# Kernel tuning notes

Hardware: AMD Instinct MI355X
Metric: run time of the kernel (lower is better)

The kernel has to match this reference:

```python
import jax, jax.numpy as jnp
import numpy as np

RAY_START, RAY_END, BOX_SIZE = 0.0, 1.0, 2.0
EPS = 1e-10


def grid_sample_bilinear(img, grid):
    """Replicates F.grid_sample(mode='bilinear', padding_mode='zeros', align_corners=True).
    img: [N, F, H, W]; grid: [N, P, 2] with (x, y) in [-1, 1] (x indexes W, y indexes H).
    Returns [N, F, P]."""
    H, W = img.shape[2], img.shape[3]
    x = (grid[..., 0] + 1.0) * 0.5 * (W - 1)  # [N, P]
    y = (grid[..., 1] + 1.0) * 0.5 * (H - 1)
    x0 = jnp.floor(x).astype(jnp.int32)
    y0 = jnp.floor(y).astype(jnp.int32)
    x1, y1 = x0 + 1, y0 + 1
    wx = x - x0.astype(x.dtype)
    wy = y - y0.astype(y.dtype)

    def gather(ix, iy):
        valid = ((ix >= 0) & (ix < W) & (iy >= 0) & (iy < H)).astype(img.dtype)
        ixc = jnp.clip(ix, 0, W - 1)
        iyc = jnp.clip(iy, 0, H - 1)
        v = jax.vmap(lambda im, jx, jy: im[:, jy, jx])(img, ixc, iyc)  # [N, F, P]
        return v * valid[:, None, :]

    return (gather(x0, y0) * ((1 - wx) * (1 - wy))[:, None, :]
            + gather(x1, y0) * (wx * (1 - wy))[:, None, :]
            + gather(x0, y1) * ((1 - wx) * wy)[:, None, :]
            + gather(x1, y1) * (wx * wy)[:, None, :])


def setup_inputs() -> dict:
    key = jax.random.key(0)
    ks = jax.random.split(key, 6)
    B, R, N, F, HP, HID = 2, 4096, 48, 32, 256, 64
    planes = jax.random.normal(ks[0], (B, 3, F, HP, HP), jnp.float32)
    ray_origins = jax.random.normal(ks[1], (B, R, 3), jnp.float32) * 0.05
    rd = jax.random.normal(ks[2], (B, R, 3), jnp.float32)
    ray_directions = rd / jnp.linalg.norm(rd, axis=-1, keepdims=True)
    jitter = jax.random.uniform(ks[3], (B, R, N, 1), jnp.float32)
    W1 = jax.random.normal(ks[4], (F, HID), jnp.float32) * 0.1
    b1 = jnp.zeros((HID,), jnp.float32)
    W2 = jax.random.normal(ks[5], (HID, 4), jnp.float32) * 0.1
    b2 = jnp.zeros((4,), jnp.float32)
    return dict(planes=planes, ray_origins=ray_origins, ray_directions=ray_directions,
                jitter=jitter, W1=W1, b1=b1, W2=W2, b2=b2)


def reference(planes, ray_origins, ray_directions, jitter, W1, b1, W2, b2):
    B, R, N, _ = jitter.shape
    F_, HP, WP = planes.shape[2], planes.shape[3], planes.shape[4]
    P = R * N

    # sample_stratified over normalized s in [0, 1], jittered (EG3D style)
    steps = jnp.arange(N, dtype=jnp.float32) / (N - 1)          # [N]
    s_delta = 1.0 / (N - 1)
    sdist = steps.reshape(1, 1, N, 1) + jitter * s_delta         # [B, R, N, 1]
    tdist = sdist * RAY_END + (1.0 - sdist) * RAY_START          # s_to_t

    # world-space sample coordinates -> tri-plane lookup
    coords = ray_origins[:, :, None, :] + tdist * ray_directions[:, :, None, :]  # [B,R,N,3]
    coords = coords.reshape(B, P, 3) / (BOX_SIZE / 2.0)
    c2d = jnp.stack([coords[..., (0, 1)], coords[..., (0, 2)], coords[..., (1, 2)]],
                    axis=1).reshape(B * 3, P, 2)
    feats = grid_sample_bilinear(planes.reshape(B * 3, F_, HP, WP), c2d)  # [B*3, F, P]
    feats = feats.reshape(B, 3, F_, P).transpose(0, 1, 3, 2)              # [B, 3, P, F]

    # OSGDecoder-style MLP: mean over planes, Linear -> softplus -> Linear
    x = feats.mean(axis=1)                      # [B, P, F]
    h = jax.nn.softplus(x @ W1 + b1)            # [B, P, HID]
    o = h @ W2 + b2                             # [B, P, 4]
    sigma = o[..., :1].reshape(B, R, N, 1)
    rgb = (jax.nn.sigmoid(o[..., 1:]) * 1.002 - 0.001).reshape(B, R, N, 3)

    # ClassicalRayMarcher (clamp_mode='softplus', cut_quantile=0, use_inf_depth=True)
    deltas = sdist[:, :, 1:] - sdist[:, :, :-1]
    deltas = jnp.concatenate([deltas, jnp.full_like(deltas[:, :, :1], 1e10)], axis=2)
    dens = jax.nn.softplus(sigma)
    alphas = 1.0 - jnp.exp(-deltas * dens)                     # [B, R, N, 1]
    T = jnp.cumprod(1.0 - alphas + EPS, axis=2)
    T = jnp.concatenate([jnp.ones_like(T[:, :, :1]), T], axis=2)  # [B, R, N+1, 1]
    final_transmittance = T[:, :, -1, 0]                       # [B, R]
    weights = alphas * T[:, :, :-1]                            # [B, R, N, 1]
    rgb_final = jnp.sum(weights * rgb, axis=2)                 # [B, R, 3]
    depth = jnp.sum(weights * sdist, axis=2)                   # [B, R, 1]
    return rgb_final, depth, weights.sum(axis=2), final_transmittance
```

## Files before the change

kernel.cpp:

```cpp
#include <hip/hip_runtime.h>
#include <math.h>

#define BATCH 2
#define RAYS  4096
#define NS    48
#define FEAT  32
#define HP    256
#define HID   64
#define NRAY  (BATCH*RAYS)
#define NSAMP (NRAY*NS)
#define S_DELTA (1.0f/47.0f)

typedef unsigned short u16;
typedef __attribute__((ext_vector_type(8))) short bfrag8;
typedef __attribute__((ext_vector_type(4))) float facc4;

__device__ __forceinline__ float softplus_f(float t) {
    float e = __expf(-fabsf(t));
    return fmaxf(t, 0.0f) + __logf(1.0f + e);
}
__device__ __forceinline__ float sigmoid_f(float t) {
    return 1.0f / (1.0f + __expf(-t));
}
__device__ __forceinline__ unsigned rtne16(float f) {
    unsigned u = __float_as_uint(f);
    return (u + 0x7FFFu + ((u >> 16) & 1u)) >> 16;
}

__global__ __launch_bounds__(256)
void prep_kernel(const float* __restrict__ planes,
                 const float* __restrict__ W1,
                 const float* __restrict__ W2,
                 u16* __restrict__ pT,
                 u16* __restrict__ W1F,
                 u16* __restrict__ W2F) {
    int idx = blockIdx.x * 256 + threadIdx.x;
    const int total = BATCH * 3 * HP * HP;
    if (idx < total) {
        int xy = idx % (HP * HP);
        int bp = idx / (HP * HP);
        const float* src = planes + (size_t)bp * FEAT * HP * HP + xy;
        unsigned o16[16];
        #pragma unroll
        for (int k = 0; k < 16; ++k) {
            float v0 = src[(size_t)(2 * k) * HP * HP];
            float v1 = src[(size_t)(2 * k + 1) * HP * HP];
            o16[k] = rtne16(v0) | (rtne16(v1) << 16);
        }
        uint4* dst = (uint4*)(pT + (size_t)idx * FEAT);
        #pragma unroll
        for (int q = 0; q < 4; ++q)
            dst[q] = make_uint4(o16[4*q], o16[4*q+1], o16[4*q+2], o16[4*q+3]);
    } else {
        int r = idx - total;
        #pragma unroll
        for (int i = 0; i < 8; ++i) {
            int e = r * 8 + i;
            int nt = e >> 9, ll = (e >> 3) & 63, ii = e & 7;
            int k = ((ll >> 4) << 3) + ii;
            int nn = (nt << 4) + (ll & 15);
            W1F[e] = (u16)rtne16(W1[k * HID + nn]);
        }
        if (r < 128) {
            #pragma unroll
            for (int i = 0; i < 8; ++i) {
                int e = r * 8 + i;
                int kk = e >> 9, ll = (e >> 3) & 63, ii = e & 7;
                int k = kk * 32 + ((ll >> 4) << 3) + ii;
                int nn = ll & 15;
                W2F[e] = (nn < 4) ? (u16)rtne16(W2[k * 4 + nn]) : (u16)0;
            }
        }
    }
}

__device__ __forceinline__ void corner_bf16(const u16* __restrict__ p,
                                            float w, float acc[8]) {
    uint4 q = *(const uint4*)p;
    unsigned uu[4] = {q.x, q.y, q.z, q.w};
    #pragma unroll
    for (int i = 0; i < 4; ++i) {
        float lo = __uint_as_float(uu[i] << 16);
        float hi = __uint_as_float(uu[i] & 0xFFFF0000u);
        acc[2*i]   = fmaf(w, lo, acc[2*i]);
        acc[2*i+1] = fmaf(w, hi, acc[2*i+1]);
    }
}

__device__ __forceinline__ void gather_plane_bf16(const u16* __restrict__ pb,
                                                  float gx, float gy, int fc8,
                                                  float acc[8]) {
    float px = (gx + 1.0f) * 0.5f * (float)(HP - 1);
    float py = (gy + 1.0f) * 0.5f * (float)(HP - 1);
    float fx = floorf(px), fy = floorf(py);
    float wx = px - fx, wy = py - fy;
    int x0 = (int)fx, y0 = (int)fy;
    int x1 = x0 + 1, y1 = y0 + 1;
    bool vx0 = (unsigned)x0 < HP, vx1 = (unsigned)x1 < HP;
    bool vy0 = (unsigned)y0 < HP, vy1 = (unsigned)y1 < HP;
    int cx0 = min(max(x0, 0), HP-1), cx1 = min(max(x1, 0), HP-1);
    int cy0 = min(max(y0, 0), HP-1), cy1 = min(max(y1, 0), HP-1);
    float w00 = (vx0 && vy0) ? (1.f-wx)*(1.f-wy) : 0.f;
    float w10 = (vx1 && vy0) ? wx*(1.f-wy)       : 0.f;
    float w01 = (vx0 && vy1) ? (1.f-wx)*wy       : 0.f;
    float w11 = (vx1 && vy1) ? wx*wy             : 0.f;
    corner_bf16(pb + ((size_t)(cy0*HP + cx0)*FEAT + fc8), w00, acc);
    corner_bf16(pb + ((size_t)(cy0*HP + cx1)*FEAT + fc8), w10, acc);
    corner_bf16(pb + ((size_t)(cy1*HP + cx0)*FEAT + fc8), w01, acc);
    corner_bf16(pb + ((size_t)(cy1*HP + cx1)*FEAT + fc8), w11, acc);
}

__global__ __launch_bounds__(256)
void sample_mlp_mfma(const u16* __restrict__ pT,
                     const float* __restrict__ rayo,
                     const float* __restrict__ rayd,
                     const float* __restrict__ jitter,
                     const u16* __restrict__ W1F,
                     const u16* __restrict__ W2F,
                     const float* __restrict__ b1,
                     const float* __restrict__ b2,
                     float4* __restrict__ smp, float* __restrict__ sds) {
    __shared__ __align__(16) u16 hlds[4][1024];
    const int t = threadIdx.x;
    const int w = t >> 6;
    const int l = t & 63;
    const int c = l & 15;
    const int g = l >> 4;
    const int sbase = (blockIdx.x * 4 + w) * 16;
    const int s = sbase + c;
    const int ray = s / NS;
    const int n = s - ray * NS;
    const int b = ray >> 12;

    const float jit = jitter[s];
    const float sd = fmaf((float)n, S_DELTA, jit * S_DELTA);
    const float ox = rayo[ray*3+0], oy = rayo[ray*3+1], oz = rayo[ray*3+2];
    const float dx = rayd[ray*3+0], dy = rayd[ray*3+1], dz = rayd[ray*3+2];
    const float cxv = fmaf(sd, dx, ox);
    const float cyv = fmaf(sd, dy, oy);
    const float czv = fmaf(sd, dz, oz);

    float acc[8];
    #pragma unroll
    for (int i = 0; i < 8; ++i) acc[i] = 0.f;

    const int fc8 = g * 8;
    const u16* base = pT + (size_t)b * 3 * HP * HP * FEAT;
    gather_plane_bf16(base,                         cxv, cyv, fc8, acc);
    gather_plane_bf16(base + (size_t)HP*HP*FEAT,    cxv, czv, fc8, acc);
    gather_plane_bf16(base + 2*(size_t)HP*HP*FEAT,  cyv, czv, fc8, acc);

    union { unsigned u[4]; bfrag8 v; } A;
    #pragma unroll
    for (int p = 0; p < 4; ++p)
        A.u[p] = rtne16(acc[2*p] * (1.f/3.f)) |
                 (rtne16(acc[2*p+1] * (1.f/3.f)) << 16);

    const facc4 z4 = {0.f, 0.f, 0.f, 0.f};
    facc4 H[4];
    #pragma unroll
    for (int nt = 0; nt < 4; ++nt) {
        union { uint4 q; bfrag8 v; } B;
        B.q = *(const uint4*)(W1F + (size_t)(nt * 64 + l) * 8);
        H[nt] = __builtin_amdgcn_mfma_f32_16x16x32_bf16(A.v, B.v, z4, 0, 0, 0);
    }

    char* lb = (char*)&hlds[w][0];
    #pragma unroll
    for (int nt = 0; nt < 4; ++nt) {
        const float bb = b1[nt * 16 + c];
        #pragma unroll
        for (int r = 0; r < 4; ++r) {
            const int row = g * 4 + r;
            const float hv = softplus_f(H[nt][r] + bb);
            const int off = row * 128 + ((((nt * 16 + c) * 2)) ^ ((row & 7) << 4));
            *(u16*)(lb + off) = (u16)rtne16(hv);
        }
    }

    facc4 O = z4;
    #pragma unroll
    for (int kk = 0; kk < 2; ++kk) {
        union { uint4 q; bfrag8 v; } A2;
        const int off = c * 128 + ((kk * 64 + g * 16) ^ ((c & 7) << 4));
        A2.q = *(const uint4*)(lb + off);
        union { uint4 q; bfrag8 v; } B2;
        B2.q = *(const uint4*)(W2F + (size_t)(kk * 64 + l) * 8);
        O = __builtin_amdgcn_mfma_f32_16x16x32_bf16(A2.v, B2.v, O, 0, 0, 0);
    }

    if (c < 4) {
        const float bb = b2[c];
        #pragma unroll
        for (int r = 0; r < 4; ++r) {
            const int ss = sbase + g * 4 + r;
            const float o = O[r] + bb;
            const float val = (c == 0) ? softplus_f(o)
                                       : (sigmoid_f(o) * 1.002f - 0.001f);
            ((float*)&smp[ss])[c] = val;
        }
    }
    if (g == 0) sds[s] = sd;
}

__global__ __launch_bounds__(256)
void composite(const float4* __restrict__ smp, const float* __restrict__ sds,
               float* __restrict__ out) {
    int w    = threadIdx.x >> 6;
    int lane = threadIdx.x & 63;
    int ray  = blockIdx.x * 4 + w;
    int base = ray * NS;
    bool valid = lane < NS;

    float4 v = make_float4(0.f, 0.f, 0.f, 0.f);
    float sd = 0.f;
    if (valid) { v = smp[base + lane]; sd = sds[base + lane]; }
    float sdn = __shfl_down(sd, 1);

    float alpha = 0.f, l = 0.f;
    if (valid) {
        float delta = (lane < NS - 1) ? (sdn - sd) : 1e10f;
        float tt = __expf(-delta * v.x);
        alpha = 1.0f - tt;
        l = __logf(tt + 1e-10f);
    }
    float sacc = l;
    #pragma unroll
    for (int off = 1; off < 64; off <<= 1) {
        float u = __shfl_up(sacc, off);
        if (lane >= off) sacc += u;
    }
    float finalLog = __shfl(sacc, NS - 1);
    float T   = __expf(sacc - l);
    float wgt = valid ? alpha * T : 0.f;

    float rf = wgt * v.y, gf = wgt * v.z, bf = wgt * v.w;
    float dep = wgt * sd, wsum = wgt;
    #pragma unroll
    for (int off = 32; off; off >>= 1) {
        rf   += __shfl_xor(rf, off);
        gf   += __shfl_xor(gf, off);
        bf   += __shfl_xor(bf, off);
        dep  += __shfl_xor(dep, off);
        wsum += __shfl_xor(wsum, off);
    }
    if (lane == 0) {
        out[ray * 3 + 0] = rf;
        out[ray * 3 + 1] = gf;
        out[ray * 3 + 2] = bf;
        out[NRAY * 3 + ray] = dep;
        out[NRAY * 4 + ray] = wsum;
        out[NRAY * 5 + ray] = __expf(finalLog);
    }
}

__global__ __launch_bounds__(192)
void render_fused(const float* __restrict__ pl,
                  const float* __restrict__ rayo,
                  const float* __restrict__ rayd,
                  const float* __restrict__ jitter,
                  const float* __restrict__ W1, const float* __restrict__ b1,
                  const float* __restrict__ W2, const float* __restrict__ b2,
                  float* __restrict__ out) {
    __shared__ float4 smpb[192];
    __shared__ float  sdsb[192];
    int tid = threadIdx.x;
    int lr  = tid / NS;
    int n   = tid - lr * NS;
    int ray = blockIdx.x * 4 + lr;
    int b   = ray >> 12;

    float jit = jitter[ray * NS + n];
    float sd  = (float)n * S_DELTA + jit * S_DELTA;
    float ox = rayo[ray*3+0], oy = rayo[ray*3+1], oz = rayo[ray*3+2];
    float dx = rayd[ray*3+0], dy = rayd[ray*3+1], dz = rayd[ray*3+2];
    float cx = fmaf(sd, dx, ox), cy = fmaf(sd, dy, oy), cz = fmaf(sd, dz, oz);

    float xv[32];
    #pragma unroll
    for (int i = 0; i < 32; ++i) xv[i] = 0.f;
    const size_t psz = (size_t)HP * HP * FEAT;
    const float* base = pl + (size_t)b * 3 * psz;
    float gxs[3] = {cx, cx, cy}, gys[3] = {cy, cz, cz};
    for (int p = 0; p < 3; ++p) {
        float px = (gxs[p] + 1.0f) * 0.5f * (float)(HP - 1);
        float py = (gys[p] + 1.0f) * 0.5f * (float)(HP - 1);
        float fx = floorf(px), fy = floorf(py);
        float wx = px - fx, wy = py - fy;
        int x0 = (int)fx, y0 = (int)fy, x1 = x0 + 1, y1 = y0 + 1;
        const float* pb = base + p * psz;
        float ws[4] = {(1.f-wx)*(1.f-wy), wx*(1.f-wy), (1.f-wx)*wy, wx*wy};
        int xs[4] = {x0, x1, x0, x1}, ys[4] = {y0, y0, y1, y1};
        for (int q = 0; q < 4; ++q) {
            if ((unsigned)xs[q] < HP && (unsigned)ys[q] < HP) {
                const float* pp = pb + (size_t)ys[q] * HP + xs[q];
                #pragma unroll
                for (int f = 0; f < 32; ++f)
                    xv[f] = fmaf(ws[q], pp[(size_t)f * HP * HP], xv[f]);
            }
        }
    }
    #pragma unroll
    for (int i = 0; i < 32; ++i) xv[i] *= (1.f/3.f);

    float o0 = b2[0], o1 = b2[1], o2 = b2[2], o3 = b2[3];
    #pragma unroll
    for (int j = 0; j < HID; ++j) {
        float hj = b1[j];
        #pragma unroll
        for (int f = 0; f < FEAT; ++f) hj = fmaf(xv[f], W1[f * HID + j], hj);
        hj = softplus_f(hj);
        o0 = fmaf(hj, W2[j*4+0], o0);
        o1 = fmaf(hj, W2[j*4+1], o1);
        o2 = fmaf(hj, W2[j*4+2], o2);
        o3 = fmaf(hj, W2[j*4+3], o3);
    }
    smpb[tid] = make_float4(softplus_f(o0),
                            sigmoid_f(o1) * 1.002f - 0.001f,
                            sigmoid_f(o2) * 1.002f - 0.001f,
                            sigmoid_f(o3) * 1.002f - 0.001f);
    sdsb[tid] = sd;
    __syncthreads();

    if (tid < 4) {
        int rray = blockIdx.x * 4 + tid;
        const float4* sp  = &smpb[tid * NS];
        const float*  sdp = &sdsb[tid * NS];
        float T = 1.0f, rf = 0.f, gf = 0.f, bfv = 0.f, dep = 0.f, wsum = 0.f;
        for (int m = 0; m < NS; ++m) {
            float4 vv = sp[m];
            float sdc = sdp[m];
            float delta = (m < NS - 1) ? (sdp[m+1] - sdc) : 1e10f;
            float alpha = 1.0f - __expf(-delta * vv.x);
            float wq = alpha * T;
            rf = fmaf(wq, vv.y, rf);
            gf = fmaf(wq, vv.z, gf);
            bfv = fmaf(wq, vv.w, bfv);
            dep = fmaf(wq, sdc, dep);
            wsum += wq;
            T *= (1.0f - alpha + 1e-10f);
        }
        out[rray*3+0] = rf;
        out[rray*3+1] = gf;
        out[rray*3+2] = bfv;
        out[NRAY*3 + rray] = dep;
        out[NRAY*4 + rray] = wsum;
        out[NRAY*5 + rray] = T;
    }
}

extern "C" void kernel_launch(void* const* d_in, const int* in_sizes, int n_in,
                              void* d_out, int out_size, void* d_ws, size_t ws_size,
                              hipStream_t stream) {
    const float* planes = (const float*)d_in[0];
    const float* rayo   = (const float*)d_in[1];
    const float* rayd   = (const float*)d_in[2];
    const float* jitter = (const float*)d_in[3];
    const float* W1     = (const float*)d_in[4];
    const float* b1     = (const float*)d_in[5];
    const float* W2     = (const float*)d_in[6];
    const float* b2     = (const float*)d_in[7];
    float* out = (float*)d_out;

    const size_t pT_bytes = (size_t)BATCH * 3 * HP * HP * FEAT * 2;
    const size_t w1f_off  = pT_bytes;
    const size_t w2f_off  = w1f_off + FEAT * HID * 2;
    const size_t smp_off  = w2f_off + HID * 16 * 2;
    const size_t sds_off  = smp_off + (size_t)NSAMP * 16;
    const size_t need     = sds_off + (size_t)NSAMP * 4;

    if (ws_size >= need) {
        char* ws = (char*)d_ws;
        u16*    pT  = (u16*)ws;
        u16*    W1F = (u16*)(ws + w1f_off);
        u16*    W2F = (u16*)(ws + w2f_off);
        float4* smp = (float4*)(ws + smp_off);
        float*  sds = (float*)(ws + sds_off);
        const int tgrid = BATCH * 3 * HP * HP / 256 + 1;
        hipLaunchKernelGGL(prep_kernel, dim3(tgrid), dim3(256), 0, stream,
                           planes, W1, W2, pT, W1F, W2F);
        hipLaunchKernelGGL(sample_mlp_mfma, dim3(NSAMP / 64), dim3(256), 0, stream,
                           pT, rayo, rayd, jitter, W1F, W2F, b1, b2, smp, sds);
        hipLaunchKernelGGL(composite, dim3(NRAY / 4), dim3(256), 0, stream,
                           smp, sds, out);
    } else {
        hipLaunchKernelGGL(render_fused, dim3(NRAY / 4), dim3(192), 0, stream,
                           planes, rayo, rayd, jitter, W1, b1, W2, b2, out);
    }
}
```

Baseline: 64.64 us.

## Fuse sampling MLP and compositing into one kernel with packed FMA gather

Merges the sample+MLP kernel and the compositing kernel into one 768-thread block that handles 4 rays (192 samples), keeping per-sample outputs in shared memory instead of a global workspace round trip. This removes one kernel launch and the write and re-read of the intermediate sample buffer. The bilinear gather accumulation now uses v_pk_fma_f32 inline asm on float pairs. In exchange there is a block-wide barrier, only 4 of the 12 waves do the compositing while the rest sit idle, and the larger block with the launch bound may limit registers and occupancy.

```diff
diff --git a/kernel.cpp b/kernel.cpp
--- a/kernel.cpp
+++ b/kernel.cpp
@@ -14,6 +14,7 @@
 typedef unsigned short u16;
 typedef __attribute__((ext_vector_type(8))) short bfrag8;
 typedef __attribute__((ext_vector_type(4))) float facc4;
+typedef __attribute__((ext_vector_type(2))) float f32x2;
 
 __device__ __forceinline__ float softplus_f(float t) {
     float e = __expf(-fabsf(t));
@@ -25,6 +26,9 @@
 __device__ __forceinline__ unsigned rtne16(float f) {
     unsigned u = __float_as_uint(f);
     return (u + 0x7FFFu + ((u >> 16) & 1u)) >> 16;
+}
+__device__ __forceinline__ void pk_fma(f32x2& d, f32x2 a, f32x2 b) {
+    asm("v_pk_fma_f32 %0, %1, %2, %0" : "+v"(d) : "v"(a), "v"(b));
 }
 
 __global__ __launch_bounds__(256)
@@ -75,21 +79,22 @@
 }
 
 __device__ __forceinline__ void corner_bf16(const u16* __restrict__ p,
-                                            float w, float acc[8]) {
+                                            float w, f32x2 acc[4]) {
     uint4 q = *(const uint4*)p;
     unsigned uu[4] = {q.x, q.y, q.z, q.w};
+    f32x2 w2 = {w, w};
     #pragma unroll
     for (int i = 0; i < 4; ++i) {
-        float lo = __uint_as_float(uu[i] << 16);
-        float hi = __uint_as_float(uu[i] & 0xFFFF0000u);
-        acc[2*i]   = fmaf(w, lo, acc[2*i]);
-        acc[2*i+1] = fmaf(w, hi, acc[2*i+1]);
+        f32x2 t;
+        t.x = __uint_as_float(uu[i] << 16);
+        t.y = __uint_as_float(uu[i] & 0xFFFF0000u);
+        pk_fma(acc[i], t, w2);
     }
 }
 
 __device__ __forceinline__ void gather_plane_bf16(const u16* __restrict__ pb,
                                                   float gx, float gy, int fc8,
-                                                  float acc[8]) {
+                                                  f32x2 acc[4]) {
     float px = (gx + 1.0f) * 0.5f * (float)(HP - 1);
     float py = (gy + 1.0f) * 0.5f * (float)(HP - 1);
     float fx = floorf(px), fy = floorf(py);
@@ -110,24 +115,28 @@
     corner_bf16(pb + ((size_t)(cy1*HP + cx1)*FEAT + fc8), w11, acc);
 }
 
-__global__ __launch_bounds__(256)
-void sample_mlp_mfma(const u16* __restrict__ pT,
-                     const float* __restrict__ rayo,
-                     const float* __restrict__ rayd,
-                     const float* __restrict__ jitter,
-                     const u16* __restrict__ W1F,
-                     const u16* __restrict__ W2F,
-                     const float* __restrict__ b1,
-                     const float* __restrict__ b2,
-                     float4* __restrict__ smp, float* __restrict__ sds) {
-    __shared__ __align__(16) u16 hlds[4][1024];
+__global__ __launch_bounds__(768, 6)
+void render_mfma(const u16* __restrict__ pT,
+                 const float* __restrict__ rayo,
+                 const float* __restrict__ rayd,
+                 const float* __restrict__ jitter,
+                 const u16* __restrict__ W1F,
+                 const u16* __restrict__ W2F,
+                 const float* __restrict__ b1,
+                 const float* __restrict__ b2,
+                 float* __restrict__ out) {
+    __shared__ __align__(16) u16 hlds[12][1024];
+    __shared__ __align__(16) float4 s_smp[192];
+    __shared__ float s_sd[192];
+
     const int t = threadIdx.x;
     const int w = t >> 6;
     const int l = t & 63;
     const int c = l & 15;
     const int g = l >> 4;
-    const int sbase = (blockIdx.x * 4 + w) * 16;
-    const int s = sbase + c;
+    const int S0 = blockIdx.x * 192;
+    const int ls = w * 16 + c;
+    const int s  = S0 + ls;
     const int ray = s / NS;
     const int n = s - ray * NS;
     const int b = ray >> 12;
@@ -140,9 +149,9 @@
     const float cyv = fmaf(sd, dy, oy);
     const float czv = fmaf(sd, dz, oz);
 
-    float acc[8];
-    #pragma unroll
-    for (int i = 0; i < 8; ++i) acc[i] = 0.f;
+    f32x2 acc[4];
+    #pragma unroll
+    for (int i = 0; i < 4; ++i) acc[i] = (f32x2){0.f, 0.f};
 
     const int fc8 = g * 8;
     const u16* base = pT + (size_t)b * 3 * HP * HP * FEAT;
@@ -153,8 +162,8 @@
     union { unsigned u[4]; bfrag8 v; } A;
     #pragma unroll
     for (int p = 0; p < 4; ++p)
-        A.u[p] = rtne16(acc[2*p] * (1.f/3.f)) |
-                 (rtne16(acc[2*p+1] * (1.f/3.f)) << 16);
+        A.u[p] = rtne16(acc[p].x * (1.f/3.f)) |
+                 (rtne16(acc[p].y * (1.f/3.f)) << 16);
 
     const facc4 z4 = {0.f, 0.f, 0.f, 0.f};
     facc4 H[4];
@@ -193,64 +202,59 @@
         const float bb = b2[c];
         #pragma unroll
         for (int r = 0; r < 4; ++r) {
-            const int ss = sbase + g * 4 + r;
+            const int li = w * 16 + g * 4 + r;
             const float o = O[r] + bb;
             const float val = (c == 0) ? softplus_f(o)
                                        : (sigmoid_f(o) * 1.002f - 0.001f);
-            ((float*)&smp[ss])[c] = val;
-        }
-    }
-    if (g == 0) sds[s] = sd;
-}
-
-__global__ __launch_bounds__(256)
-void composite(const float4* __restrict__ smp, const float* __restrict__ sds,
-               float* __restrict__ out) {
-    int w    = threadIdx.x >> 6;
-    int lane = threadIdx.x & 63;
-    int ray  = blockIdx.x * 4 + w;
-    int base = ray * NS;
-    bool valid = lane < NS;
-
-    float4 v = make_float4(0.f, 0.f, 0.f, 0.f);
-    float sd = 0.f;
-    if (valid) { v = smp[base + lane]; sd = sds[base + lane]; }
-    float sdn = __shfl_down(sd, 1);
-
-    float alpha = 0.f, l = 0.f;
-    if (valid) {
-        float delta = (lane < NS - 1) ? (sdn - sd) : 1e10f;
-        float tt = __expf(-delta * v.x);
-        alpha = 1.0f - tt;
-        l = __logf(tt + 1e-10f);
-    }
-    float sacc = l;
-    #pragma unroll
-    for (int off = 1; off < 64; off <<= 1) {
-        float u = __shfl_up(sacc, off);
-        if (lane >= off) sacc += u;
-    }
-    float finalLog = __shfl(sacc, NS - 1);
-    float T   = __expf(sacc - l);
-    float wgt = valid ? alpha * T : 0.f;
-
-    float rf = wgt * v.y, gf = wgt * v.z, bf = wgt * v.w;
-    float dep = wgt * sd, wsum = wgt;
-    #pragma unroll
-    for (int off = 32; off; off >>= 1) {
-        rf   += __shfl_xor(rf, off);
-        gf   += __shfl_xor(gf, off);
-        bf   += __shfl_xor(bf, off);
-        dep  += __shfl_xor(dep, off);
-        wsum += __shfl_xor(wsum, off);
-    }
-    if (lane == 0) {
-        out[ray * 3 + 0] = rf;
-        out[ray * 3 + 1] = gf;
-        out[ray * 3 + 2] = bf;
-        out[NRAY * 3 + ray] = dep;
-        out[NRAY * 4 + ray] = wsum;
-        out[NRAY * 5 + ray] = __expf(finalLog);
+            ((float*)&s_smp[li])[c] = val;
+        }
+    }
+    if (g == 0) s_sd[ls] = sd;
+    __syncthreads();
+
+    if (w < 4) {
+        const int rray = blockIdx.x * 4 + w;
+        const bool valid = l < NS;
+        float4 v = make_float4(0.f, 0.f, 0.f, 0.f);
+        float sdc = 0.f;
+        if (valid) { v = s_smp[w * NS + l]; sdc = s_sd[w * NS + l]; }
+        float sdn = __shfl_down(sdc, 1);
+
+        float alpha = 0.f, lg = 0.f;
+        if (valid) {
+            float delta = (l < NS - 1) ? (sdn - sdc) : 1e10f;
+            float tt = __expf(-delta * v.x);
+            alpha = 1.0f - tt;
+            lg = __logf(tt + 1e-10f);
+        }
+        float sacc = lg;
+        #pragma unroll
+        for (int off = 1; off < 64; off <<= 1) {
+            float u = __shfl_up(sacc, off);
+            if (l >= off) sacc += u;
+        }
+        float finalLog = __shfl(sacc, NS - 1);
+        float T   = __expf(sacc - lg);
+        float wgt = valid ? alpha * T : 0.f;
+
+        float rf = wgt * v.y, gf = wgt * v.z, bf = wgt * v.w;
+        float dep = wgt * sdc, wsum = wgt;
+        #pragma unroll
+        for (int off = 32; off; off >>= 1) {
+            rf   += __shfl_xor(rf, off);
+            gf   += __shfl_xor(gf, off);
+            bf   += __shfl_xor(bf, off);
+            dep  += __shfl_xor(dep, off);
+            wsum += __shfl_xor(wsum, off);
+        }
+        if (l == 0) {
+            out[rray * 3 + 0] = rf;
+            out[rray * 3 + 1] = gf;
+            out[rray * 3 + 2] = bf;
+            out[NRAY * 3 + rray] = dep;
+            out[NRAY * 4 + rray] = wsum;
+            out[NRAY * 5 + rray] = __expf(finalLog);
+        }
     }
 }
 
@@ -364,25 +368,19 @@
 
     const size_t pT_bytes = (size_t)BATCH * 3 * HP * HP * FEAT * 2;
     const size_t w1f_off  = pT_bytes;
-    const size_t w2f_off  = w1f_off + FEAT * HID * 2;
-    const size_t smp_off  = w2f_off + HID * 16 * 2;
-    const size_t sds_off  = smp_off + (size_t)NSAMP * 16;
-    const size_t need     = sds_off + (size_t)NSAMP * 4;
+    const size_t w2f_off  = w1f_off + (size_t)FEAT * HID * 2;
+    const size_t need     = w2f_off + (size_t)HID * 16 * 2;
 
     if (ws_size >= need) {
         char* ws = (char*)d_ws;
-        u16*    pT  = (u16*)ws;
-        u16*    W1F = (u16*)(ws + w1f_off);
-        u16*    W2F = (u16*)(ws + w2f_off);
-        float4* smp = (float4*)(ws + smp_off);
-        float*  sds = (float*)(ws + sds_off);
+        u16* pT  = (u16*)ws;
+        u16* W1F = (u16*)(ws + w1f_off);
+        u16* W2F = (u16*)(ws + w2f_off);
         const int tgrid = BATCH * 3 * HP * HP / 256 + 1;
         hipLaunchKernelGGL(prep_kernel, dim3(tgrid), dim3(256), 0, stream,
                            planes, W1, W2, pT, W1F, W2F);
-        hipLaunchKernelGGL(sample_mlp_mfma, dim3(NSAMP / 64), dim3(256), 0, stream,
-                           pT, rayo, rayd, jitter, W1F, W2F, b1, b2, smp, sds);
-        hipLaunchKernelGGL(composite, dim3(NRAY / 4), dim3(256), 0, stream,
-                           smp, sds, out);
+        hipLaunchKernelGGL(render_mfma, dim3(NSAMP / 192), dim3(768), 0, stream,
+                           pT, rayo, rayd, jitter, W1F, W2F, b1, b2, out);
     } else {
         hipLaunchKernelGGL(render_fused, dim3(NRAY / 4), dim3(192), 0, stream,
                            planes, rayo, rayd, jitter, W1, b1, W2, b2, out);
```

Result: faster. 62.67 us (-3.0%).
